# Kernel optimization log

Hardware: AMD Instinct MI355X
Metric: run time of the kernel (lower is better)

## Reference

```python
import jax, jax.numpy as jnp
import numpy as np

N, E, G = 50000, 800000, 512
HD, ED, GD, HID = 128, 64, 64, 128  # h_dim, e_dim, g_dim, hid_dim


def _mlp2(x, W1, b1, W2, b2, last_act):
    # Linear -> ReLU -> Linear (-> optional last activation)
    y = jax.nn.relu(x @ W1 + b1) @ W2 + b2
    return last_act(y) if last_act is not None else y


def setup_inputs() -> dict:
    key = jax.random.key(0)
    ks = list(jax.random.split(key, 24))
    ki = iter(ks)

    def p(shape):
        return (jax.random.normal(next(ki), shape, jnp.float32) * 0.02)

    inp = {
        "h": jax.random.normal(next(ki), (N, HD), jnp.float32),
        "e_index": jax.random.randint(next(ki), (2, E), 0, N),
        "e": jax.random.normal(next(ki), (E, ED), jnp.float32),
        "g": jax.random.normal(next(ki), (G, GD), jnp.float32),
        "batch": jnp.sort(jax.random.randint(next(ki), (N,), 0, G)),
        # fc_m: [2*HD+ED+GD, HID, HID], last_activation=relu
        "W_m1": p((2 * HD + ED + GD, HID)), "b_m1": jnp.zeros((HID,), jnp.float32),
        "W_m2": p((HID, HID)), "b_m2": jnp.zeros((HID,), jnp.float32),
        # fc_m_att: [HID, 1], sigmoid
        "W_ma": p((HID, 1)), "b_ma": jnp.zeros((1,), jnp.float32),
        # fc_e: [HID, ED, ED]
        "W_e1": p((HID, ED)), "b_e1": jnp.zeros((ED,), jnp.float32),
        "W_e2": p((ED, ED)), "b_e2": jnp.zeros((ED,), jnp.float32),
        # fc_h: [HD+HID+GD, HD, HD]
        "W_h1": p((HD + HID + GD, HD)), "b_h1": jnp.zeros((HD,), jnp.float32),
        "W_h2": p((HD, HD)), "b_h2": jnp.zeros((HD,), jnp.float32),
        # fc_h_att: [HD, 1]
        "W_ha": p((HD, 1)), "b_ha": jnp.zeros((1,), jnp.float32),
        # fc_g: [GD+HD, GD, GD]
        "W_g1": p((GD + HD, GD)), "b_g1": jnp.zeros((GD,), jnp.float32),
        "W_g2": p((GD, GD)), "b_g2": jnp.zeros((GD,), jnp.float32),
    }
    return inp


def reference(h, e_index, e, g, batch,
              W_m1, b_m1, W_m2, b_m2, W_ma, b_ma,
              W_e1, b_e1, W_e2, b_e2,
              W_h1, b_h1, W_h2, b_h2, W_ha, b_ha,
              W_g1, b_g1, W_g2, b_g2):
    src, dst = e_index[0], e_index[1]
    e_batch = batch[dst]

    # edge message: concat gathered endpoints + edge feat + gathered global
    m_cat = jnp.concatenate([h[src], h[dst], e, g[e_batch]], axis=1)  # [E, 2HD+ED+GD]
    m = jax.nn.relu(jax.nn.relu(m_cat @ W_m1 + b_m1) @ W_m2 + b_m2)   # [E, HID]
    m_att = jax.nn.sigmoid(m @ W_ma + b_ma)                            # [E, 1]

    e_update = _mlp2(m, W_e1, b_e1, W_e2, b_e2, None)                  # [E, ED]
    e_out = jax.nn.relu(e + e_update)

    m_aggr = jax.ops.segment_sum(m_att * m, dst, num_segments=h.shape[0])  # [N, HID]

    h_cat = jnp.concatenate([h, m_aggr, g[batch]], axis=1)             # [N, HD+HID+GD]
    h_update = _mlp2(h_cat, W_h1, b_h1, W_h2, b_h2, None)
    h_out = jax.nn.relu(h + h_update)                                  # [N, HD]
    h_att = h_out @ W_ha + b_ha                                        # [N, 1]

    h_aggr = jax.ops.segment_sum(h_att * h_out, batch, num_segments=g.shape[0])  # [G, HD]

    g_cat = jnp.concatenate([g, h_aggr], axis=1)                       # [G, GD+HD]
    g_update = _mlp2(g_cat, W_g1, b_g1, W_g2, b_g2, None)
    g_out = jax.nn.relu(g + g_update)

    return (h_out, e_out, g_out)
```

## Files before the change

### kernel.cpp

```cpp
#include <hip/hip_runtime.h>
#include <hip/hip_bf16.h>

#define NN 50000
#define NE 800000
#define NG 512
#define HD 128
#define ED 64
#define GD 64
#define HID 128

typedef __attribute__((ext_vector_type(8))) short short8;
typedef __attribute__((ext_vector_type(4))) short short4v;
typedef __attribute__((ext_vector_type(4))) float f32x4;

__device__ __forceinline__ short f2bf(float f) {
  union { float f; unsigned u; } v; v.f = f;
  unsigned r = v.u + 0x7fffu + ((v.u >> 16) & 1u);
  return (short)(r >> 16);
}

__device__ __forceinline__ float bf2f(short s) {
  union { unsigned u; float f; } v;
  v.u = ((unsigned)(unsigned short)s) << 16;
  return v.f;
}

__device__ __forceinline__ short8 load_a8(const float* p) {
  const f32x4* q = (const f32x4*)p;
  f32x4 x0 = q[0], x1 = q[1];
  short8 r;
  r[0]=f2bf(x0[0]); r[1]=f2bf(x0[1]); r[2]=f2bf(x0[2]); r[3]=f2bf(x0[3]);
  r[4]=f2bf(x1[0]); r[5]=f2bf(x1[1]); r[6]=f2bf(x1[2]); r[7]=f2bf(x1[3]);
  return r;
}

__device__ __forceinline__ int swz(int row, int col, int rowBytes) {
  int b = row * rowBytes + col * 2;
  b ^= (row & 7) << 4;
  return b >> 1;
}

__global__ void pack_kernel(const float* __restrict__ Wm1, const float* __restrict__ Wm2,
                            const float* __restrict__ We1, const float* __restrict__ We2,
                            const float* __restrict__ Wh1, const float* __restrict__ Wh2,
                            short* __restrict__ out) {
  int gid = blockIdx.x * 256 + threadIdx.x;
  if (gid >= 135168) return;
  const float* W; int Ncol, base, idx;
  if (gid < 49152)       { W = Wm1; Ncol = 128; base = 0;      idx = gid; }
  else if (gid < 65536)  { W = Wm2; Ncol = 128; base = 49152;  idx = gid - 49152; }
  else if (gid < 73728)  { W = We1; Ncol = 64;  base = 65536;  idx = gid - 65536; }
  else if (gid < 77824)  { W = We2; Ncol = 64;  base = 73728;  idx = gid - 73728; }
  else if (gid < 118784) { W = Wh1; Ncol = 128; base = 77824;  idx = gid - 77824; }
  else                   { W = Wh2; Ncol = 128; base = 118784; idx = gid - 118784; }
  int k = idx / Ncol, n = idx % Ncol;
  out[base + (k >> 3) * Ncol * 8 + n * 8 + (k & 7)] = f2bf(W[idx]);
}

__global__ void cast_kernel(const float* __restrict__ h, const float* __restrict__ g,
                            short* __restrict__ h_bf, short* __restrict__ g_bf) {
  int gid = blockIdx.x * 256 + threadIdx.x;
  const int H4 = NN * HD / 4;
  const int G4 = NG * GD / 4;
  if (gid < H4) {
    f32x4 v = ((const f32x4*)h)[gid];
    short4v r; r[0]=f2bf(v[0]); r[1]=f2bf(v[1]); r[2]=f2bf(v[2]); r[3]=f2bf(v[3]);
    *(short4v*)(h_bf + gid * 4) = r;
  } else if (gid < H4 + G4) {
    int i = gid - H4;
    f32x4 v = ((const f32x4*)g)[i];
    short4v r; r[0]=f2bf(v[0]); r[1]=f2bf(v[1]); r[2]=f2bf(v[2]); r[3]=f2bf(v[3]);
    *(short4v*)(g_bf + i * 4) = r;
  }
}

__global__ void count_kernel(const int* __restrict__ ei, int* __restrict__ deg) {
  int i = blockIdx.x * 256 + threadIdx.x;
  if (i < NE) atomicAdd(&deg[ei[NE + i]], 1);
}

__global__ __launch_bounds__(1024) void scan_kernel(int* __restrict__ deg) {
  __shared__ int psum[1024];
  const int CH = 49;
  int t = threadIdx.x;
  int lo = t * CH, hi = lo + CH; if (hi > NN) hi = NN; if (lo > NN) lo = NN;
  int s = 0;
  for (int i = lo; i < hi; ++i) s += deg[i];
  psum[t] = s;
  __syncthreads();
  for (int d = 1; d < 1024; d <<= 1) {
    int v = (t >= d) ? psum[t - d] : 0;
    __syncthreads();
    psum[t] += v;
    __syncthreads();
  }
  int run = (t == 0) ? 0 : psum[t - 1];
  for (int i = lo; i < hi; ++i) { int v = deg[i]; deg[i] = run; run += v; }
}

__global__ void scatter_kernel(const int* __restrict__ ei, int* __restrict__ off,
                               int* __restrict__ elist) {
  int i = blockIdx.x * 256 + threadIdx.x;
  if (i < NE) {
    int d = ei[NE + i];
    int p = atomicAdd(&off[d], 1);
    elist[p] = i;
  }
}

__global__ __launch_bounds__(256) void edge_kernel(
    const short* __restrict__ h_bf, const int* __restrict__ ei,
    const float* __restrict__ e, const short* __restrict__ g_bf,
    const int* __restrict__ batch, const int* __restrict__ elist,
    const short* __restrict__ pWm1, const float* __restrict__ bm1,
    const short* __restrict__ pWm2, const float* __restrict__ bm2,
    const float* __restrict__ Wma, const float* __restrict__ bma,
    const short* __restrict__ pWe1, const float* __restrict__ be1,
    const short* __restrict__ pWe2, const float* __restrict__ be2,
    float* __restrict__ e_out, float* __restrict__ m_aggr) {
  __shared__ short lds_m[4][16 * 128];
  __shared__ short lds_t[4][16 * 64];
  __shared__ int sdst[64];

  const int wave = threadIdx.x >> 6;
  const int lane = threadIdx.x & 63;
  const int row16 = lane & 15;
  const int quad = lane >> 4;
  const int pbase = blockIdx.x * 64 + wave * 16;

  const int eidA = elist[pbase + row16];
  const int srcA = ei[eidA];
  const int dstA = ei[NE + eidA];
  const int gbA = batch[dstA];
  if (quad == 0) sdst[wave * 16 + row16] = dstA;

  int eidS[4];
#pragma unroll
  for (int r = 0; r < 4; ++r) eidS[r] = elist[pbase + quad * 4 + r];

  short8 afr[12];
  {
    const short* s0 = h_bf + (size_t)srcA * HD;
    const short* s1 = h_bf + (size_t)dstA * HD;
    const float* s2 = e + (size_t)eidA * ED;
    const short* s3 = g_bf + (size_t)gbA * GD;
#pragma unroll
    for (int c = 0; c < 4; ++c) afr[c] = *(const short8*)(s0 + c * 32 + quad * 8);
#pragma unroll
    for (int c = 0; c < 4; ++c) afr[4 + c] = *(const short8*)(s1 + c * 32 + quad * 8);
    afr[8] = load_a8(s2 + quad * 8);
    afr[9] = load_a8(s2 + 32 + quad * 8);
    afr[10] = *(const short8*)(s3 + quad * 8);
    afr[11] = *(const short8*)(s3 + 32 + quad * 8);
  }

  float eres[4][4];
#pragma unroll
  for (int t = 0; t < 4; ++t)
#pragma unroll
    for (int r = 0; r < 4; ++r)
      eres[t][r] = e[(size_t)eidS[r] * ED + t * 16 + row16];

  f32x4 acc[8];
#pragma unroll
  for (int t = 0; t < 8; ++t) acc[t] = (f32x4)0.0f;
#pragma unroll
  for (int c = 0; c < 12; ++c) {
    const short* bp = pWm1 + (size_t)(c * 4 + quad) * HID * 8 + row16 * 8;
#pragma unroll
    for (int t = 0; t < 8; ++t) {
      short8 b = *(const short8*)(bp + t * 16 * 8);
      acc[t] = __builtin_amdgcn_mfma_f32_16x16x32_bf16(afr[c], b, acc[t], 0, 0, 0);
    }
  }
#pragma unroll
  for (int t = 0; t < 8; ++t) {
    float b1 = bm1[t * 16 + row16];
#pragma unroll
    for (int r = 0; r < 4; ++r) {
      float y = fmaxf(acc[t][r] + b1, 0.f);
      lds_m[wave][swz(quad * 4 + r, t * 16 + row16, 256)] = f2bf(y);
    }
  }

  f32x4 acc2[8];
#pragma unroll
  for (int t = 0; t < 8; ++t) acc2[t] = (f32x4)0.0f;
#pragma unroll
  for (int c = 0; c < 4; ++c) {
    short8 a = *(const short8*)&lds_m[wave][swz(row16, c * 32 + quad * 8, 256)];
    const short* bp = pWm2 + (size_t)(c * 4 + quad) * HID * 8 + row16 * 8;
#pragma unroll
    for (int t = 0; t < 8; ++t) {
      short8 b = *(const short8*)(bp + t * 16 * 8);
      acc2[t] = __builtin_amdgcn_mfma_f32_16x16x32_bf16(a, b, acc2[t], 0, 0, 0);
    }
  }

  float mval[8][4];
#pragma unroll
  for (int t = 0; t < 8; ++t) {
    float b2 = bm2[t * 16 + row16];
#pragma unroll
    for (int r = 0; r < 4; ++r) {
      float y = fmaxf(acc2[t][r] + b2, 0.f);
      mval[t][r] = y;
      lds_m[wave][swz(quad * 4 + r, t * 16 + row16, 256)] = f2bf(y);
    }
  }

  float part[4] = {0.f, 0.f, 0.f, 0.f};
#pragma unroll
  for (int t = 0; t < 8; ++t) {
    float w = Wma[t * 16 + row16];
#pragma unroll
    for (int r = 0; r < 4; ++r) part[r] += mval[t][r] * w;
  }
#pragma unroll
  for (int s = 1; s < 16; s <<= 1) {
#pragma unroll
    for (int r = 0; r < 4; ++r) part[r] += __shfl_xor(part[r], s, 64);
  }
  float bma0 = bma[0];
  float attv[4];
#pragma unroll
  for (int r = 0; r < 4; ++r) attv[r] = 1.f / (1.f + __expf(-(part[r] + bma0)));

  f32x4 acc3[4];
#pragma unroll
  for (int t = 0; t < 4; ++t) acc3[t] = (f32x4)0.0f;
#pragma unroll
  for (int c = 0; c < 4; ++c) {
    short8 a = *(const short8*)&lds_m[wave][swz(row16, c * 32 + quad * 8, 256)];
    const short* bp = pWe1 + (size_t)(c * 4 + quad) * ED * 8 + row16 * 8;
#pragma unroll
    for (int t = 0; t < 4; ++t) {
      short8 b = *(const short8*)(bp + t * 16 * 8);
      acc3[t] = __builtin_amdgcn_mfma_f32_16x16x32_bf16(a, b, acc3[t], 0, 0, 0);
    }
  }
#pragma unroll
  for (int t = 0; t < 4; ++t) {
    float b1 = be1[t * 16 + row16];
#pragma unroll
    for (int r = 0; r < 4; ++r) {
      float y = fmaxf(acc3[t][r] + b1, 0.f);
      lds_t[wave][swz(quad * 4 + r, t * 16 + row16, 128)] = f2bf(y);
    }
  }

#pragma unroll
  for (int t = 0; t < 8; ++t)
#pragma unroll
    for (int r = 0; r < 4; ++r)
      lds_m[wave][swz(quad * 4 + r, t * 16 + row16, 256)] = f2bf(attv[r] * mval[t][r]);

  f32x4 acc4[4];
#pragma unroll
  for (int t = 0; t < 4; ++t) acc4[t] = (f32x4)0.0f;
#pragma unroll
  for (int c = 0; c < 2; ++c) {
    short8 a = *(const short8*)&lds_t[wave][swz(row16, c * 32 + quad * 8, 128)];
    const short* bp = pWe2 + (size_t)(c * 4 + quad) * ED * 8 + row16 * 8;
#pragma unroll
    for (int t = 0; t < 4; ++t) {
      short8 b = *(const short8*)(bp + t * 16 * 8);
      acc4[t] = __builtin_amdgcn_mfma_f32_16x16x32_bf16(a, b, acc4[t], 0, 0, 0);
    }
  }
#pragma unroll
  for (int t = 0; t < 4; ++t) {
    float b2 = be2[t * 16 + row16];
#pragma unroll
    for (int r = 0; r < 4; ++r) {
      int col = t * 16 + row16;
      float v = eres[t][r] + acc4[t][r] + b2;
      e_out[(size_t)eidS[r] * ED + col] = fmaxf(v, 0.f);
    }
  }

  __syncthreads();

  {
    int col = threadIdx.x & 127;
    int r0 = (threadIdx.x >> 7) * 32;
    int cur = sdst[r0];
    float sum = 0.f;
    bool first = true;
#pragma unroll 1
    for (int r = r0; r < r0 + 32; ++r) {
      int d = sdst[r];
      float v = bf2f(lds_m[r >> 4][swz(r & 15, col, 256)]);
      if (d != cur) {
        if (first) atomicAdd(&m_aggr[(size_t)cur * HID + col], sum);
        else m_aggr[(size_t)cur * HID + col] = sum;
        first = false; cur = d; sum = v;
      } else {
        sum += v;
      }
    }
    atomicAdd(&m_aggr[(size_t)cur * HID + col], sum);
  }
}

__global__ __launch_bounds__(256) void node_kernel(
    const float* __restrict__ h, const short* __restrict__ h_bf,
    const float* __restrict__ m_aggr, const short* __restrict__ g_bf,
    const int* __restrict__ batch,
    const short* __restrict__ pWh1, const float* __restrict__ bh1,
    const short* __restrict__ pWh2, const float* __restrict__ bh2,
    const float* __restrict__ Wha, const float* __restrict__ bha,
    float* __restrict__ h_out, float* __restrict__ h_aggr) {
  __shared__ short lds_y[4][16 * 128];
  __shared__ int sbat[64];

  const int wave = threadIdx.x >> 6;
  const int lane = threadIdx.x & 63;
  const int row16 = lane & 15;
  const int quad = lane >> 4;
  const int nbase = blockIdx.x * 64 + wave * 16;

  int nA = nbase + row16;
  int nAc = nA < NN ? nA : NN - 1;
  int gbA = batch[nAc];
  if (quad == 0) sbat[wave * 16 + row16] = (nA < NN) ? gbA : -1;

  short8 afr[10];
  {
    const short* s0 = h_bf + (size_t)nAc * HD;
    const float* s1 = m_aggr + (size_t)nAc * HID;
    const short* s2 = g_bf + (size_t)gbA * GD;
#pragma unroll
    for (int c = 0; c < 4; ++c) afr[c] = *(const short8*)(s0 + c * 32 + quad * 8);
#pragma unroll
    for (int c = 0; c < 4; ++c) afr[4 + c] = load_a8(s1 + c * 32 + quad * 8);
    afr[8] = *(const short8*)(s2 + quad * 8);
    afr[9] = *(const short8*)(s2 + 32 + quad * 8);
  }

  f32x4 acc[8];
#pragma unroll
  for (int t = 0; t < 8; ++t) acc[t] = (f32x4)0.0f;
#pragma unroll
  for (int c = 0; c < 10; ++c) {
    const short* bp = pWh1 + (size_t)(c * 4 + quad) * HD * 8 + row16 * 8;
#pragma unroll
    for (int t = 0; t < 8; ++t) {
      short8 b = *(const short8*)(bp + t * 16 * 8);
      acc[t] = __builtin_amdgcn_mfma_f32_16x16x32_bf16(afr[c], b, acc[t], 0, 0, 0);
    }
  }
#pragma unroll
  for (int t = 0; t < 8; ++t) {
    float b1 = bh1[t * 16 + row16];
#pragma unroll
    for (int r = 0; r < 4; ++r) {
      float y = fmaxf(acc[t][r] + b1, 0.f);
      lds_y[wave][swz(quad * 4 + r, t * 16 + row16, 256)] = f2bf(y);
    }
  }

  f32x4 acc2[8];
#pragma unroll
  for (int t = 0; t < 8; ++t) acc2[t] = (f32x4)0.0f;
#pragma unroll
  for (int c = 0; c < 4; ++c) {
    short8 a = *(const short8*)&lds_y[wave][swz(row16, c * 32 + quad * 8, 256)];
    const short* bp = pWh2 + (size_t)(c * 4 + quad) * HD * 8 + row16 * 8;
#pragma unroll
    for (int t = 0; t < 8; ++t) {
      short8 b = *(const short8*)(bp + t * 16 * 8);
      acc2[t] = __builtin_amdgcn_mfma_f32_16x16x32_bf16(a, b, acc2[t], 0, 0, 0);
    }
  }

  float hval[8][4];
  int nS[4];
#pragma unroll
  for (int r = 0; r < 4; ++r) nS[r] = nbase + quad * 4 + r;
#pragma unroll
  for (int t = 0; t < 8; ++t) {
    float b2 = bh2[t * 16 + row16];
#pragma unroll
    for (int r = 0; r < 4; ++r) {
      float v = 0.f;
      if (nS[r] < NN) {
        v = h[(size_t)nS[r] * HD + t * 16 + row16] + acc2[t][r] + b2;
        v = fmaxf(v, 0.f);
        h_out[(size_t)nS[r] * HD + t * 16 + row16] = v;
      }
      hval[t][r] = v;
    }
  }

  float part[4] = {0.f, 0.f, 0.f, 0.f};
#pragma unroll
  for (int t = 0; t < 8; ++t) {
    float w = Wha[t * 16 + row16];
#pragma unroll
    for (int r = 0; r < 4; ++r) part[r] += hval[t][r] * w;
  }
#pragma unroll
  for (int s = 1; s < 16; s <<= 1) {
#pragma unroll
    for (int r = 0; r < 4; ++r) part[r] += __shfl_xor(part[r], s, 64);
  }
  float bha0 = bha[0];
#pragma unroll
  for (int t = 0; t < 8; ++t)
#pragma unroll
    for (int r = 0; r < 4; ++r)
      lds_y[wave][swz(quad * 4 + r, t * 16 + row16, 256)] =
          f2bf((part[r] + bha0) * hval[t][r]);

  __syncthreads();

  {
    int col = threadIdx.x & 127;
    int r0 = (threadIdx.x >> 7) * 32;
    int cur = sbat[r0];
    float sum = 0.f;
    bool first = true;
#pragma unroll 1
    for (int r = r0; r < r0 + 32; ++r) {
      int d = sbat[r];
      float v = bf2f(lds_y[r >> 4][swz(r & 15, col, 256)]);
      if (d != cur) {
        if (cur >= 0) {
          if (first) atomicAdd(&h_aggr[(size_t)cur * HD + col], sum);
          else h_aggr[(size_t)cur * HD + col] = sum;
        }
        first = false; cur = d; sum = v;
      } else {
        sum += v;
      }
    }
    if (cur >= 0) atomicAdd(&h_aggr[(size_t)cur * HD + col], sum);
  }
}

__global__ void g_kernel(const float* __restrict__ g, const float* __restrict__ h_aggr,
                         const float* __restrict__ Wg1, const float* __restrict__ bg1,
                         const float* __restrict__ Wg2, const float* __restrict__ bg2,
                         float* __restrict__ g_out) {
  __shared__ float cat[192];
  __shared__ float y1[64];
  int r = blockIdx.x;
  int t = threadIdx.x;
  cat[t] = g[(size_t)r * GD + t];
  cat[64 + t] = h_aggr[(size_t)r * HD + t];
  cat[128 + t] = h_aggr[(size_t)r * HD + 64 + t];
  __syncthreads();
  float a = bg1[t];
  for (int k = 0; k < 192; ++k) a += cat[k] * Wg1[k * 64 + t];
  y1[t] = fmaxf(a, 0.f);
  __syncthreads();
  float b = bg2[t];
  for (int k = 0; k < 64; ++k) b += y1[k] * Wg2[k * 64 + t];
  float v = g[(size_t)r * GD + t] + b;
  g_out[(size_t)r * GD + t] = fmaxf(v, 0.f);
}

extern "C" void kernel_launch(void* const* d_in, const int* in_sizes, int n_in,
                              void* d_out, int out_size, void* d_ws, size_t ws_size,
                              hipStream_t stream) {
  const float* h = (const float*)d_in[0];
  const int* ei = (const int*)d_in[1];
  const float* e = (const float*)d_in[2];
  const float* g = (const float*)d_in[3];
  const int* batch = (const int*)d_in[4];
  const float* Wm1 = (const float*)d_in[5];
  const float* bm1 = (const float*)d_in[6];
  const float* Wm2 = (const float*)d_in[7];
  const float* bm2 = (const float*)d_in[8];
  const float* Wma = (const float*)d_in[9];
  const float* bma = (const float*)d_in[10];
  const float* We1 = (const float*)d_in[11];
  const float* be1 = (const float*)d_in[12];
  const float* We2 = (const float*)d_in[13];
  const float* be2 = (const float*)d_in[14];
  const float* Wh1 = (const float*)d_in[15];
  const float* bh1 = (const float*)d_in[16];
  const float* Wh2 = (const float*)d_in[17];
  const float* bh2 = (const float*)d_in[18];
  const float* Wha = (const float*)d_in[19];
  const float* bha = (const float*)d_in[20];
  const float* Wg1 = (const float*)d_in[21];
  const float* bg1 = (const float*)d_in[22];
  const float* Wg2 = (const float*)d_in[23];
  const float* bg2 = (const float*)d_in[24];

  float* out = (float*)d_out;
  float* h_out = out;
  float* e_out = out + (size_t)NN * HD;
  float* g_out = e_out + (size_t)NE * ED;

  char* ws = (char*)d_ws;
  float* m_aggr = (float*)ws;
  float* h_aggr = (float*)(ws + 25600000);
  short* packed = (short*)(ws + 25862144);
  int* deg      = (int*)(ws + 26132480);
  int* elist    = (int*)(ws + 26332480);
  short* h_bf   = (short*)(ws + 29532480);
  short* g_bf   = (short*)(ws + 42332480);
  short* pWm1 = packed;
  short* pWm2 = packed + 49152;
  short* pWe1 = packed + 65536;
  short* pWe2 = packed + 73728;
  short* pWh1 = packed + 77824;
  short* pWh2 = packed + 118784;

  hipMemsetAsync(m_aggr, 0, (size_t)NN * HID * 4, stream);
  hipMemsetAsync(h_aggr, 0, (size_t)NG * HD * 4, stream);
  hipMemsetAsync(deg, 0, (size_t)NN * 4, stream);

  pack_kernel<<<(135168 + 255) / 256, 256, 0, stream>>>(Wm1, Wm2, We1, We2, Wh1, Wh2, packed);
  cast_kernel<<<(1608192 + 255) / 256, 256, 0, stream>>>(h, g, h_bf, g_bf);
  count_kernel<<<(NE + 255) / 256, 256, 0, stream>>>(ei, deg);
  scan_kernel<<<1, 1024, 0, stream>>>(deg);
  scatter_kernel<<<(NE + 255) / 256, 256, 0, stream>>>(ei, deg, elist);

  edge_kernel<<<NE / 64, 256, 0, stream>>>(h_bf, ei, e, g_bf, batch, elist,
                                           pWm1, bm1, pWm2, bm2, Wma, bma,
                                           pWe1, be1, pWe2, be2, e_out, m_aggr);

  node_kernel<<<(NN + 63) / 64, 256, 0, stream>>>(h, h_bf, m_aggr, g_bf, batch,
                                                  pWh1, bh1, pWh2, bh2, Wha, bha,
                                                  h_out, h_aggr);

  g_kernel<<<NG, 64, 0, stream>>>(g, h_aggr, Wg1, bg1, Wg2, bg2, g_out);
}
```

Baseline: 728.7 us.

## Retile edge kernel to 256 edges per block with 32x32 MFMA

Rewrites the edge kernel to process 256 edges per block, each wave covering 64 rows with 32x32x16 bf16 MFMAs instead of 16x16x32. This lets each weight fragment loaded from memory feed two row tiles, which reduces weight traffic per edge. Attention scaling moves into the segment-sum pass, which now runs over 128-row runs and so issues fewer atomics. The second e-MLP layer is deferred until after the aggregation, reusing the same LDS buffer. The cost is much higher register pressure (a launch bound of 2 blocks) and a larger LDS footprint per block, which may reduce occupancy.

```diff
diff --git a/kernel.cpp b/kernel.cpp
--- a/kernel.cpp
+++ b/kernel.cpp
@@ -8,10 +8,12 @@
 #define ED 64
 #define GD 64
 #define HID 128
+#define EB 256
 
 typedef __attribute__((ext_vector_type(8))) short short8;
 typedef __attribute__((ext_vector_type(4))) short short4v;
 typedef __attribute__((ext_vector_type(4))) float f32x4;
+typedef __attribute__((ext_vector_type(16))) float f32x16;
 
 __device__ __forceinline__ short f2bf(float f) {
   union { float f; unsigned u; } v; v.f = f;
@@ -108,7 +110,7 @@
   }
 }
 
-__global__ __launch_bounds__(256) void edge_kernel(
+__global__ __launch_bounds__(256, 2) void edge_kernel(
     const short* __restrict__ h_bf, const int* __restrict__ ei,
     const float* __restrict__ e, const short* __restrict__ g_bf,
     const int* __restrict__ batch, const int* __restrict__ elist,
@@ -118,179 +120,176 @@
     const short* __restrict__ pWe1, const float* __restrict__ be1,
     const short* __restrict__ pWe2, const float* __restrict__ be2,
     float* __restrict__ e_out, float* __restrict__ m_aggr) {
-  __shared__ short lds_m[4][16 * 128];
-  __shared__ short lds_t[4][16 * 64];
-  __shared__ int sdst[64];
-
-  const int wave = threadIdx.x >> 6;
-  const int lane = threadIdx.x & 63;
-  const int row16 = lane & 15;
-  const int quad = lane >> 4;
-  const int pbase = blockIdx.x * 64 + wave * 16;
-
-  const int eidA = elist[pbase + row16];
-  const int srcA = ei[eidA];
-  const int dstA = ei[NE + eidA];
-  const int gbA = batch[dstA];
-  if (quad == 0) sdst[wave * 16 + row16] = dstA;
-
-  int eidS[4];
-#pragma unroll
-  for (int r = 0; r < 4; ++r) eidS[r] = elist[pbase + quad * 4 + r];
-
-  short8 afr[12];
+  __shared__ short lds_m[EB * 128];
+  __shared__ float att_s[EB];
+  __shared__ int sdst[EB];
+  __shared__ int seid[EB];
+  short* ebuf = lds_m;
+
+  const int tid = threadIdx.x;
+  const int w = tid >> 6;
+  const int l = tid & 63;
+  const int c32 = l & 31;
+  const int hi = l >> 5;
+  const int eb = blockIdx.x * EB;
+
   {
-    const short* s0 = h_bf + (size_t)srcA * HD;
-    const short* s1 = h_bf + (size_t)dstA * HD;
-    const float* s2 = e + (size_t)eidA * ED;
-    const short* s3 = g_bf + (size_t)gbA * GD;
-#pragma unroll
-    for (int c = 0; c < 4; ++c) afr[c] = *(const short8*)(s0 + c * 32 + quad * 8);
-#pragma unroll
-    for (int c = 0; c < 4; ++c) afr[4 + c] = *(const short8*)(s1 + c * 32 + quad * 8);
-    afr[8] = load_a8(s2 + quad * 8);
-    afr[9] = load_a8(s2 + 32 + quad * 8);
-    afr[10] = *(const short8*)(s3 + quad * 8);
-    afr[11] = *(const short8*)(s3 + 32 + quad * 8);
-  }
-
-  float eres[4][4];
-#pragma unroll
-  for (int t = 0; t < 4; ++t)
-#pragma unroll
-    for (int r = 0; r < 4; ++r)
-      eres[t][r] = e[(size_t)eidS[r] * ED + t * 16 + row16];
-
-  f32x4 acc[8];
-#pragma unroll
-  for (int t = 0; t < 8; ++t) acc[t] = (f32x4)0.0f;
-#pragma unroll
-  for (int c = 0; c < 12; ++c) {
-    const short* bp = pWm1 + (size_t)(c * 4 + quad) * HID * 8 + row16 * 8;
-#pragma unroll
-    for (int t = 0; t < 8; ++t) {
-      short8 b = *(const short8*)(bp + t * 16 * 8);
-      acc[t] = __builtin_amdgcn_mfma_f32_16x16x32_bf16(afr[c], b, acc[t], 0, 0, 0);
-    }
-  }
-#pragma unroll
-  for (int t = 0; t < 8; ++t) {
-    float b1 = bm1[t * 16 + row16];
-#pragma unroll
-    for (int r = 0; r < 4; ++r) {
-      float y = fmaxf(acc[t][r] + b1, 0.f);
-      lds_m[wave][swz(quad * 4 + r, t * 16 + row16, 256)] = f2bf(y);
-    }
-  }
-
-  f32x4 acc2[8];
-#pragma unroll
-  for (int t = 0; t < 8; ++t) acc2[t] = (f32x4)0.0f;
-#pragma unroll
-  for (int c = 0; c < 4; ++c) {
-    short8 a = *(const short8*)&lds_m[wave][swz(row16, c * 32 + quad * 8, 256)];
-    const short* bp = pWm2 + (size_t)(c * 4 + quad) * HID * 8 + row16 * 8;
-#pragma unroll
-    for (int t = 0; t < 8; ++t) {
-      short8 b = *(const short8*)(bp + t * 16 * 8);
-      acc2[t] = __builtin_amdgcn_mfma_f32_16x16x32_bf16(a, b, acc2[t], 0, 0, 0);
-    }
-  }
-
-  float mval[8][4];
-#pragma unroll
-  for (int t = 0; t < 8; ++t) {
-    float b2 = bm2[t * 16 + row16];
-#pragma unroll
-    for (int r = 0; r < 4; ++r) {
-      float y = fmaxf(acc2[t][r] + b2, 0.f);
-      mval[t][r] = y;
-      lds_m[wave][swz(quad * 4 + r, t * 16 + row16, 256)] = f2bf(y);
-    }
-  }
-
-  float part[4] = {0.f, 0.f, 0.f, 0.f};
-#pragma unroll
-  for (int t = 0; t < 8; ++t) {
-    float w = Wma[t * 16 + row16];
-#pragma unroll
-    for (int r = 0; r < 4; ++r) part[r] += mval[t][r] * w;
-  }
-#pragma unroll
-  for (int s = 1; s < 16; s <<= 1) {
-#pragma unroll
-    for (int r = 0; r < 4; ++r) part[r] += __shfl_xor(part[r], s, 64);
-  }
-  float bma0 = bma[0];
-  float attv[4];
-#pragma unroll
-  for (int r = 0; r < 4; ++r) attv[r] = 1.f / (1.f + __expf(-(part[r] + bma0)));
-
-  f32x4 acc3[4];
-#pragma unroll
-  for (int t = 0; t < 4; ++t) acc3[t] = (f32x4)0.0f;
-#pragma unroll
-  for (int c = 0; c < 4; ++c) {
-    short8 a = *(const short8*)&lds_m[wave][swz(row16, c * 32 + quad * 8, 256)];
-    const short* bp = pWe1 + (size_t)(c * 4 + quad) * ED * 8 + row16 * 8;
+    int eid = elist[eb + tid];
+    seid[tid] = eid;
+    sdst[tid] = ei[NE + eid];
+  }
+
+  int eidr[2], srcr[2], dstr[2], gbr[2];
+#pragma unroll
+  for (int rt = 0; rt < 2; ++rt) {
+    int row = w * 64 + rt * 32 + c32;
+    int eid = seid[row];
+    eidr[rt] = eid;
+    dstr[rt] = sdst[row];
+    srcr[rt] = ei[eid];
+    gbr[rt] = batch[dstr[rt]];
+  }
+
+  f32x16 acc[2][4];
+#pragma unroll
+  for (int rt = 0; rt < 2; ++rt)
+#pragma unroll
+    for (int t = 0; t < 4; ++t) acc[rt][t] = (f32x16)0.0f;
+
+#pragma unroll
+  for (int kk = 0; kk < 24; ++kk) {
+    short8 a[2];
+#pragma unroll
+    for (int rt = 0; rt < 2; ++rt) {
+      if (kk < 8)
+        a[rt] = *(const short8*)(h_bf + (size_t)srcr[rt] * HD + kk * 16 + hi * 8);
+      else if (kk < 16)
+        a[rt] = *(const short8*)(h_bf + (size_t)dstr[rt] * HD + (kk - 8) * 16 + hi * 8);
+      else if (kk < 20)
+        a[rt] = load_a8(e + (size_t)eidr[rt] * ED + (kk - 16) * 16 + hi * 8);
+      else
+        a[rt] = *(const short8*)(g_bf + (size_t)gbr[rt] * GD + (kk - 20) * 16 + hi * 8);
+    }
+    const short* bp = pWm1 + (size_t)(kk * 2 + hi) * (HID * 8) + c32 * 8;
 #pragma unroll
     for (int t = 0; t < 4; ++t) {
-      short8 b = *(const short8*)(bp + t * 16 * 8);
-      acc3[t] = __builtin_amdgcn_mfma_f32_16x16x32_bf16(a, b, acc3[t], 0, 0, 0);
-    }
-  }
-#pragma unroll
-  for (int t = 0; t < 4; ++t) {
-    float b1 = be1[t * 16 + row16];
-#pragma unroll
-    for (int r = 0; r < 4; ++r) {
-      float y = fmaxf(acc3[t][r] + b1, 0.f);
-      lds_t[wave][swz(quad * 4 + r, t * 16 + row16, 128)] = f2bf(y);
-    }
-  }
-
-#pragma unroll
-  for (int t = 0; t < 8; ++t)
-#pragma unroll
-    for (int r = 0; r < 4; ++r)
-      lds_m[wave][swz(quad * 4 + r, t * 16 + row16, 256)] = f2bf(attv[r] * mval[t][r]);
-
-  f32x4 acc4[4];
-#pragma unroll
-  for (int t = 0; t < 4; ++t) acc4[t] = (f32x4)0.0f;
-#pragma unroll
-  for (int c = 0; c < 2; ++c) {
-    short8 a = *(const short8*)&lds_t[wave][swz(row16, c * 32 + quad * 8, 128)];
-    const short* bp = pWe2 + (size_t)(c * 4 + quad) * ED * 8 + row16 * 8;
+      short8 b = *(const short8*)(bp + t * 32 * 8);
+#pragma unroll
+      for (int rt = 0; rt < 2; ++rt)
+        acc[rt][t] = __builtin_amdgcn_mfma_f32_32x32x16_bf16(a[rt], b, acc[rt][t], 0, 0, 0);
+    }
+  }
+
+#pragma unroll
+  for (int rt = 0; rt < 2; ++rt)
 #pragma unroll
     for (int t = 0; t < 4; ++t) {
-      short8 b = *(const short8*)(bp + t * 16 * 8);
-      acc4[t] = __builtin_amdgcn_mfma_f32_16x16x32_bf16(a, b, acc4[t], 0, 0, 0);
-    }
-  }
-#pragma unroll
-  for (int t = 0; t < 4; ++t) {
-    float b2 = be2[t * 16 + row16];
-#pragma unroll
-    for (int r = 0; r < 4; ++r) {
-      int col = t * 16 + row16;
-      float v = eres[t][r] + acc4[t][r] + b2;
-      e_out[(size_t)eidS[r] * ED + col] = fmaxf(v, 0.f);
+      float bb = bm1[t * 32 + c32];
+#pragma unroll
+      for (int q = 0; q < 16; ++q) {
+        int row = w * 64 + rt * 32 + (q & 3) + 8 * (q >> 2) + 4 * hi;
+        float y = fmaxf(acc[rt][t][q] + bb, 0.f);
+        lds_m[swz(row, t * 32 + c32, 256)] = f2bf(y);
+      }
+    }
+
+  f32x16 acc2[2][4];
+#pragma unroll
+  for (int rt = 0; rt < 2; ++rt)
+#pragma unroll
+    for (int t = 0; t < 4; ++t) acc2[rt][t] = (f32x16)0.0f;
+
+#pragma unroll
+  for (int ks = 0; ks < 8; ++ks) {
+    short8 a[2];
+#pragma unroll
+    for (int rt = 0; rt < 2; ++rt)
+      a[rt] = *(const short8*)&lds_m[swz(w * 64 + rt * 32 + c32, ks * 16 + hi * 8, 256)];
+    const short* bp = pWm2 + (size_t)(ks * 2 + hi) * (HID * 8) + c32 * 8;
+#pragma unroll
+    for (int t = 0; t < 4; ++t) {
+      short8 b = *(const short8*)(bp + t * 32 * 8);
+#pragma unroll
+      for (int rt = 0; rt < 2; ++rt)
+        acc2[rt][t] = __builtin_amdgcn_mfma_f32_32x32x16_bf16(a[rt], b, acc2[rt][t], 0, 0, 0);
+    }
+  }
+
+  float p[2][16];
+#pragma unroll
+  for (int rt = 0; rt < 2; ++rt)
+#pragma unroll
+    for (int q = 0; q < 16; ++q) p[rt][q] = 0.f;
+
+#pragma unroll
+  for (int rt = 0; rt < 2; ++rt)
+#pragma unroll
+    for (int t = 0; t < 4; ++t) {
+      float bb = bm2[t * 32 + c32];
+      float wv = Wma[t * 32 + c32];
+#pragma unroll
+      for (int q = 0; q < 16; ++q) {
+        int row = w * 64 + rt * 32 + (q & 3) + 8 * (q >> 2) + 4 * hi;
+        float y = fmaxf(acc2[rt][t][q] + bb, 0.f);
+        lds_m[swz(row, t * 32 + c32, 256)] = f2bf(y);
+        p[rt][q] += y * wv;
+      }
+    }
+
+#pragma unroll
+  for (int s = 1; s <= 16; s <<= 1) {
+#pragma unroll
+    for (int rt = 0; rt < 2; ++rt)
+#pragma unroll
+      for (int q = 0; q < 16; ++q) p[rt][q] += __shfl_xor(p[rt][q], s, 64);
+  }
+  {
+    float bma0 = bma[0];
+    if (c32 == 0) {
+#pragma unroll
+      for (int rt = 0; rt < 2; ++rt)
+#pragma unroll
+        for (int q = 0; q < 16; ++q) {
+          int row = w * 64 + rt * 32 + (q & 3) + 8 * (q >> 2) + 4 * hi;
+          att_s[row] = 1.f / (1.f + __expf(-(p[rt][q] + bma0)));
+        }
+    }
+  }
+
+  f32x16 acc3[2][2];
+#pragma unroll
+  for (int rt = 0; rt < 2; ++rt)
+#pragma unroll
+    for (int t = 0; t < 2; ++t) acc3[rt][t] = (f32x16)0.0f;
+
+#pragma unroll
+  for (int ks = 0; ks < 8; ++ks) {
+    short8 a[2];
+#pragma unroll
+    for (int rt = 0; rt < 2; ++rt)
+      a[rt] = *(const short8*)&lds_m[swz(w * 64 + rt * 32 + c32, ks * 16 + hi * 8, 256)];
+    const short* bp = pWe1 + (size_t)(ks * 2 + hi) * (ED * 8) + c32 * 8;
+#pragma unroll
+    for (int t = 0; t < 2; ++t) {
+      short8 b = *(const short8*)(bp + t * 32 * 8);
+#pragma unroll
+      for (int rt = 0; rt < 2; ++rt)
+        acc3[rt][t] = __builtin_amdgcn_mfma_f32_32x32x16_bf16(a[rt], b, acc3[rt][t], 0, 0, 0);
     }
   }
 
   __syncthreads();
 
   {
-    int col = threadIdx.x & 127;
-    int r0 = (threadIdx.x >> 7) * 32;
+    int col = tid & 127;
+    int r0 = (tid >> 7) * 128;
     int cur = sdst[r0];
     float sum = 0.f;
     bool first = true;
 #pragma unroll 1
-    for (int r = r0; r < r0 + 32; ++r) {
+    for (int r = r0; r < r0 + 128; ++r) {
       int d = sdst[r];
-      float v = bf2f(lds_m[r >> 4][swz(r & 15, col, 256)]);
+      float v = bf2f(lds_m[swz(r, col, 256)]) * att_s[r];
       if (d != cur) {
         if (first) atomicAdd(&m_aggr[(size_t)cur * HID + col], sum);
         else m_aggr[(size_t)cur * HID + col] = sum;
@@ -301,6 +300,58 @@
     }
     atomicAdd(&m_aggr[(size_t)cur * HID + col], sum);
   }
+
+  __syncthreads();
+
+#pragma unroll
+  for (int rt = 0; rt < 2; ++rt)
+#pragma unroll
+    for (int t = 0; t < 2; ++t) {
+      float bb = be1[t * 32 + c32];
+#pragma unroll
+      for (int q = 0; q < 16; ++q) {
+        int row = w * 64 + rt * 32 + (q & 3) + 8 * (q >> 2) + 4 * hi;
+        float y = fmaxf(acc3[rt][t][q] + bb, 0.f);
+        ebuf[swz(row, t * 32 + c32, 128)] = f2bf(y);
+      }
+    }
+
+  f32x16 acc4[2][2];
+#pragma unroll
+  for (int rt = 0; rt < 2; ++rt)
+#pragma unroll
+    for (int t = 0; t < 2; ++t) acc4[rt][t] = (f32x16)0.0f;
+
+#pragma unroll
+  for (int ks = 0; ks < 4; ++ks) {
+    short8 a[2];
+#pragma unroll
+    for (int rt = 0; rt < 2; ++rt)
+      a[rt] = *(const short8*)&ebuf[swz(w * 64 + rt * 32 + c32, ks * 16 + hi * 8, 128)];
+    const short* bp = pWe2 + (size_t)(ks * 2 + hi) * (ED * 8) + c32 * 8;
+#pragma unroll
+    for (int t = 0; t < 2; ++t) {
+      short8 b = *(const short8*)(bp + t * 32 * 8);
+#pragma unroll
+      for (int rt = 0; rt < 2; ++rt)
+        acc4[rt][t] = __builtin_amdgcn_mfma_f32_32x32x16_bf16(a[rt], b, acc4[rt][t], 0, 0, 0);
+    }
+  }
+
+#pragma unroll
+  for (int rt = 0; rt < 2; ++rt)
+#pragma unroll
+    for (int t = 0; t < 2; ++t) {
+      float bb = be2[t * 32 + c32];
+#pragma unroll
+      for (int q = 0; q < 16; ++q) {
+        int row = w * 64 + rt * 32 + (q & 3) + 8 * (q >> 2) + 4 * hi;
+        int eid = seid[row];
+        int col = t * 32 + c32;
+        float v = e[(size_t)eid * ED + col] + acc4[rt][t][q] + bb;
+        e_out[(size_t)eid * ED + col] = fmaxf(v, 0.f);
+      }
+    }
 }
 
 __global__ __launch_bounds__(256) void node_kernel(
@@ -520,7 +571,7 @@
   scan_kernel<<<1, 1024, 0, stream>>>(deg);
   scatter_kernel<<<(NE + 255) / 256, 256, 0, stream>>>(ei, deg, elist);
 
-  edge_kernel<<<NE / 64, 256, 0, stream>>>(h_bf, ei, e, g_bf, batch, elist,
+  edge_kernel<<<NE / EB, 256, 0, stream>>>(h_bf, ei, e, g_bf, batch, elist,
                                            pWm1, bm1, pWm2, bm2, Wma, bma,
                                            pWe1, be1, pWe2, be2, e_out, m_aggr);
 
```

Result: slower. 940.6 us (+29.1%).

## Pre-cast edge features to bf16 and slim edge kernel register and LDS use

Applied to the files above, without the earlier changes.

Edge features are now converted to bf16 in the cast kernel, which also absorbs the degree-count pass, so one launch is removed. The edge kernel no longer preloads all twelve A fragments, the fp32 residual or the m values into registers. It loads A fragments per chunk, keeps attention weights in LDS and uses a single shared LDS buffer for m and the e-MLP hidden layer, all to cut VGPR and LDS pressure and raise occupancy. The segment aggregation now runs earlier and applies attention on the fly with paired columns. The cost is an extra full pass over the edge features plus a bf16 copy written to and read back from memory. The e_out residual also now uses bf16-rounded e, which lowers accuracy.

```diff
diff --git a/kernel.cpp b/kernel.cpp
--- a/kernel.cpp
+++ b/kernel.cpp
@@ -8,9 +8,11 @@
 #define ED 64
 #define GD 64
 #define HID 128
+#define EB 64
 
 typedef __attribute__((ext_vector_type(8))) short short8;
 typedef __attribute__((ext_vector_type(4))) short short4v;
+typedef __attribute__((ext_vector_type(2))) float f32x2;
 typedef __attribute__((ext_vector_type(4))) float f32x4;
 
 __device__ __forceinline__ short f2bf(float f) {
@@ -58,10 +60,13 @@
 }
 
 __global__ void cast_kernel(const float* __restrict__ h, const float* __restrict__ g,
-                            short* __restrict__ h_bf, short* __restrict__ g_bf) {
+                            const float* __restrict__ e, const int* __restrict__ ei,
+                            short* __restrict__ h_bf, short* __restrict__ g_bf,
+                            short* __restrict__ e_bf, int* __restrict__ deg) {
   int gid = blockIdx.x * 256 + threadIdx.x;
   const int H4 = NN * HD / 4;
   const int G4 = NG * GD / 4;
+  const int E4 = NE * ED / 4;
   if (gid < H4) {
     f32x4 v = ((const f32x4*)h)[gid];
     short4v r; r[0]=f2bf(v[0]); r[1]=f2bf(v[1]); r[2]=f2bf(v[2]); r[3]=f2bf(v[3]);
@@ -71,12 +76,15 @@
     f32x4 v = ((const f32x4*)g)[i];
     short4v r; r[0]=f2bf(v[0]); r[1]=f2bf(v[1]); r[2]=f2bf(v[2]); r[3]=f2bf(v[3]);
     *(short4v*)(g_bf + i * 4) = r;
-  }
-}
-
-__global__ void count_kernel(const int* __restrict__ ei, int* __restrict__ deg) {
-  int i = blockIdx.x * 256 + threadIdx.x;
-  if (i < NE) atomicAdd(&deg[ei[NE + i]], 1);
+  } else if (gid < H4 + G4 + E4) {
+    int i = gid - H4 - G4;
+    f32x4 v = ((const f32x4*)e)[i];
+    short4v r; r[0]=f2bf(v[0]); r[1]=f2bf(v[1]); r[2]=f2bf(v[2]); r[3]=f2bf(v[3]);
+    *(short4v*)(e_bf + i * 4) = r;
+  } else if (gid < H4 + G4 + E4 + NE) {
+    int i = gid - H4 - G4 - E4;
+    atomicAdd(&deg[ei[NE + i]], 1);
+  }
 }
 
 __global__ __launch_bounds__(1024) void scan_kernel(int* __restrict__ deg) {
@@ -110,7 +118,7 @@
 
 __global__ __launch_bounds__(256) void edge_kernel(
     const short* __restrict__ h_bf, const int* __restrict__ ei,
-    const float* __restrict__ e, const short* __restrict__ g_bf,
+    const short* __restrict__ e_bf, const short* __restrict__ g_bf,
     const int* __restrict__ batch, const int* __restrict__ elist,
     const short* __restrict__ pWm1, const float* __restrict__ bm1,
     const short* __restrict__ pWm2, const float* __restrict__ bm2,
@@ -118,59 +126,51 @@
     const short* __restrict__ pWe1, const float* __restrict__ be1,
     const short* __restrict__ pWe2, const float* __restrict__ be2,
     float* __restrict__ e_out, float* __restrict__ m_aggr) {
-  __shared__ short lds_m[4][16 * 128];
-  __shared__ short lds_t[4][16 * 64];
-  __shared__ int sdst[64];
-
-  const int wave = threadIdx.x >> 6;
-  const int lane = threadIdx.x & 63;
+  __shared__ short lds_m[EB * 128];
+  __shared__ float att_s[EB];
+  __shared__ int sdst[EB];
+  __shared__ int seid[EB];
+  short* ebuf = lds_m;
+
+  const int tid = threadIdx.x;
+  const int w = tid >> 6;
+  const int lane = tid & 63;
   const int row16 = lane & 15;
   const int quad = lane >> 4;
-  const int pbase = blockIdx.x * 64 + wave * 16;
-
-  const int eidA = elist[pbase + row16];
-  const int srcA = ei[eidA];
-  const int dstA = ei[NE + eidA];
-  const int gbA = batch[dstA];
-  if (quad == 0) sdst[wave * 16 + row16] = dstA;
-
-  int eidS[4];
-#pragma unroll
-  for (int r = 0; r < 4; ++r) eidS[r] = elist[pbase + quad * 4 + r];
-
-  short8 afr[12];
-  {
-    const short* s0 = h_bf + (size_t)srcA * HD;
-    const short* s1 = h_bf + (size_t)dstA * HD;
-    const float* s2 = e + (size_t)eidA * ED;
-    const short* s3 = g_bf + (size_t)gbA * GD;
-#pragma unroll
-    for (int c = 0; c < 4; ++c) afr[c] = *(const short8*)(s0 + c * 32 + quad * 8);
-#pragma unroll
-    for (int c = 0; c < 4; ++c) afr[4 + c] = *(const short8*)(s1 + c * 32 + quad * 8);
-    afr[8] = load_a8(s2 + quad * 8);
-    afr[9] = load_a8(s2 + 32 + quad * 8);
-    afr[10] = *(const short8*)(s3 + quad * 8);
-    afr[11] = *(const short8*)(s3 + 32 + quad * 8);
-  }
-
-  float eres[4][4];
-#pragma unroll
-  for (int t = 0; t < 4; ++t)
-#pragma unroll
-    for (int r = 0; r < 4; ++r)
-      eres[t][r] = e[(size_t)eidS[r] * ED + t * 16 + row16];
+  const int eb = blockIdx.x * EB;
+
+  if (tid < EB) {
+    int eid = elist[eb + tid];
+    seid[tid] = eid;
+    sdst[tid] = ei[NE + eid];
+  }
+
+  const int eidr = elist[eb + w * 16 + row16];
+  const int dstr = ei[NE + eidr];
+  const int srcr = ei[eidr];
+  const int gbr = batch[dstr];
+
+  const short* seg0 = h_bf + (size_t)srcr * HD;
+  const short* seg1 = h_bf + (size_t)dstr * HD;
+  const short* seg2 = e_bf + (size_t)eidr * ED;
+  const short* seg3 = g_bf + (size_t)gbr * GD;
 
   f32x4 acc[8];
 #pragma unroll
   for (int t = 0; t < 8; ++t) acc[t] = (f32x4)0.0f;
 #pragma unroll
   for (int c = 0; c < 12; ++c) {
-    const short* bp = pWm1 + (size_t)(c * 4 + quad) * HID * 8 + row16 * 8;
+    const short* src; int off;
+    if (c < 4)       { src = seg0; off = c * 32; }
+    else if (c < 8)  { src = seg1; off = (c - 4) * 32; }
+    else if (c < 10) { src = seg2; off = (c - 8) * 32; }
+    else             { src = seg3; off = (c - 10) * 32; }
+    short8 a = *(const short8*)(src + off + quad * 8);
+    const short* bp = pWm1 + (size_t)(c * 4 + quad) * (HID * 8) + row16 * 8;
 #pragma unroll
     for (int t = 0; t < 8; ++t) {
       short8 b = *(const short8*)(bp + t * 16 * 8);
-      acc[t] = __builtin_amdgcn_mfma_f32_16x16x32_bf16(afr[c], b, acc[t], 0, 0, 0);
+      acc[t] = __builtin_amdgcn_mfma_f32_16x16x32_bf16(a, b, acc[t], 0, 0, 0);
     }
   }
 #pragma unroll
@@ -179,7 +179,7 @@
 #pragma unroll
     for (int r = 0; r < 4; ++r) {
       float y = fmaxf(acc[t][r] + b1, 0.f);
-      lds_m[wave][swz(quad * 4 + r, t * 16 + row16, 256)] = f2bf(y);
+      lds_m[swz(w * 16 + quad * 4 + r, t * 16 + row16, 256)] = f2bf(y);
     }
   }
 
@@ -188,8 +188,8 @@
   for (int t = 0; t < 8; ++t) acc2[t] = (f32x4)0.0f;
 #pragma unroll
   for (int c = 0; c < 4; ++c) {
-    short8 a = *(const short8*)&lds_m[wave][swz(row16, c * 32 + quad * 8, 256)];
-    const short* bp = pWm2 + (size_t)(c * 4 + quad) * HID * 8 + row16 * 8;
+    short8 a = *(const short8*)&lds_m[swz(w * 16 + row16, c * 32 + quad * 8, 256)];
+    const short* bp = pWm2 + (size_t)(c * 4 + quad) * (HID * 8) + row16 * 8;
 #pragma unroll
     for (int t = 0; t < 8; ++t) {
       short8 b = *(const short8*)(bp + t * 16 * 8);
@@ -197,109 +197,118 @@
     }
   }
 
-  float mval[8][4];
+  float p[4] = {0.f, 0.f, 0.f, 0.f};
 #pragma unroll
   for (int t = 0; t < 8; ++t) {
     float b2 = bm2[t * 16 + row16];
+    float wv = Wma[t * 16 + row16];
 #pragma unroll
     for (int r = 0; r < 4; ++r) {
       float y = fmaxf(acc2[t][r] + b2, 0.f);
-      mval[t][r] = y;
-      lds_m[wave][swz(quad * 4 + r, t * 16 + row16, 256)] = f2bf(y);
-    }
-  }
-
-  float part[4] = {0.f, 0.f, 0.f, 0.f};
-#pragma unroll
-  for (int t = 0; t < 8; ++t) {
-    float w = Wma[t * 16 + row16];
-#pragma unroll
-    for (int r = 0; r < 4; ++r) part[r] += mval[t][r] * w;
-  }
+      lds_m[swz(w * 16 + quad * 4 + r, t * 16 + row16, 256)] = f2bf(y);
+      p[r] += y * wv;
+    }
+  }
+
 #pragma unroll
   for (int s = 1; s < 16; s <<= 1) {
 #pragma unroll
-    for (int r = 0; r < 4; ++r) part[r] += __shfl_xor(part[r], s, 64);
-  }
-  float bma0 = bma[0];
-  float attv[4];
-#pragma unroll
-  for (int r = 0; r < 4; ++r) attv[r] = 1.f / (1.f + __expf(-(part[r] + bma0)));
+    for (int r = 0; r < 4; ++r) p[r] += __shfl_xor(p[r], s, 64);
+  }
+  {
+    float bma0 = bma[0];
+    if (row16 == 0) {
+#pragma unroll
+      for (int r = 0; r < 4; ++r)
+        att_s[w * 16 + quad * 4 + r] = 1.f / (1.f + __expf(-(p[r] + bma0)));
+    }
+  }
 
   f32x4 acc3[4];
 #pragma unroll
   for (int t = 0; t < 4; ++t) acc3[t] = (f32x4)0.0f;
 #pragma unroll
   for (int c = 0; c < 4; ++c) {
-    short8 a = *(const short8*)&lds_m[wave][swz(row16, c * 32 + quad * 8, 256)];
-    const short* bp = pWe1 + (size_t)(c * 4 + quad) * ED * 8 + row16 * 8;
+    short8 a = *(const short8*)&lds_m[swz(w * 16 + row16, c * 32 + quad * 8, 256)];
+    const short* bp = pWe1 + (size_t)(c * 4 + quad) * (ED * 8) + row16 * 8;
 #pragma unroll
     for (int t = 0; t < 4; ++t) {
       short8 b = *(const short8*)(bp + t * 16 * 8);
       acc3[t] = __builtin_amdgcn_mfma_f32_16x16x32_bf16(a, b, acc3[t], 0, 0, 0);
     }
   }
+
+  __syncthreads();
+
+  {
+    int cp = tid & 63;
+    int r0 = (tid >> 6) * 16;
+    int cur = sdst[r0];
+    float s0 = 0.f, s1 = 0.f;
+    bool first = true;
+#pragma unroll 1
+    for (int r = r0; r < r0 + 16; ++r) {
+      int d = sdst[r];
+      unsigned u = *(const unsigned*)&lds_m[swz(r, cp * 2, 256)];
+      float av = att_s[r];
+      float v0 = bf2f((short)(u & 0xffffu)) * av;
+      float v1 = bf2f((short)(u >> 16)) * av;
+      if (d != cur) {
+        if (first) {
+          atomicAdd(&m_aggr[(size_t)cur * HID + cp * 2], s0);
+          atomicAdd(&m_aggr[(size_t)cur * HID + cp * 2 + 1], s1);
+        } else {
+          f32x2 st; st[0] = s0; st[1] = s1;
+          *(f32x2*)&m_aggr[(size_t)cur * HID + cp * 2] = st;
+        }
+        first = false; cur = d; s0 = v0; s1 = v1;
+      } else {
+        s0 += v0; s1 += v1;
+      }
+    }
+    atomicAdd(&m_aggr[(size_t)cur * HID + cp * 2], s0);
+    atomicAdd(&m_aggr[(size_t)cur * HID + cp * 2 + 1], s1);
+  }
+
+  __syncthreads();
+
 #pragma unroll
   for (int t = 0; t < 4; ++t) {
     float b1 = be1[t * 16 + row16];
 #pragma unroll
     for (int r = 0; r < 4; ++r) {
       float y = fmaxf(acc3[t][r] + b1, 0.f);
-      lds_t[wave][swz(quad * 4 + r, t * 16 + row16, 128)] = f2bf(y);
-    }
-  }
-
-#pragma unroll
-  for (int t = 0; t < 8; ++t)
-#pragma unroll
-    for (int r = 0; r < 4; ++r)
-      lds_m[wave][swz(quad * 4 + r, t * 16 + row16, 256)] = f2bf(attv[r] * mval[t][r]);
+      ebuf[swz(w * 16 + quad * 4 + r, t * 16 + row16, 128)] = f2bf(y);
+    }
+  }
 
   f32x4 acc4[4];
 #pragma unroll
   for (int t = 0; t < 4; ++t) acc4[t] = (f32x4)0.0f;
 #pragma unroll
   for (int c = 0; c < 2; ++c) {
-    short8 a = *(const short8*)&lds_t[wave][swz(row16, c * 32 + quad * 8, 128)];
-    const short* bp = pWe2 + (size_t)(c * 4 + quad) * ED * 8 + row16 * 8;
+    short8 a = *(const short8*)&ebuf[swz(w * 16 + row16, c * 32 + quad * 8, 128)];
+    const short* bp = pWe2 + (size_t)(c * 4 + quad) * (ED * 8) + row16 * 8;
 #pragma unroll
     for (int t = 0; t < 4; ++t) {
       short8 b = *(const short8*)(bp + t * 16 * 8);
       acc4[t] = __builtin_amdgcn_mfma_f32_16x16x32_bf16(a, b, acc4[t], 0, 0, 0);
     }
   }
+
+  int eidS[4];
+#pragma unroll
+  for (int r = 0; r < 4; ++r) eidS[r] = seid[w * 16 + quad * 4 + r];
 #pragma unroll
   for (int t = 0; t < 4; ++t) {
     float b2 = be2[t * 16 + row16];
 #pragma unroll
     for (int r = 0; r < 4; ++r) {
       int col = t * 16 + row16;
-      float v = eres[t][r] + acc4[t][r] + b2;
+      float res = bf2f(e_bf[(size_t)eidS[r] * ED + col]);
+      float v = res + acc4[t][r] + b2;
       e_out[(size_t)eidS[r] * ED + col] = fmaxf(v, 0.f);
     }
-  }
-
-  __syncthreads();
-
-  {
-    int col = threadIdx.x & 127;
-    int r0 = (threadIdx.x >> 7) * 32;
-    int cur = sdst[r0];
-    float sum = 0.f;
-    bool first = true;
-#pragma unroll 1
-    for (int r = r0; r < r0 + 32; ++r) {
-      int d = sdst[r];
-      float v = bf2f(lds_m[r >> 4][swz(r & 15, col, 256)]);
-      if (d != cur) {
-        if (first) atomicAdd(&m_aggr[(size_t)cur * HID + col], sum);
-        else m_aggr[(size_t)cur * HID + col] = sum;
-        first = false; cur = d; sum = v;
-      } else {
-        sum += v;
-      }
-    }
-    atomicAdd(&m_aggr[(size_t)cur * HID + col], sum);
   }
 }
 
@@ -503,6 +512,7 @@
   int* elist    = (int*)(ws + 26332480);
   short* h_bf   = (short*)(ws + 29532480);
   short* g_bf   = (short*)(ws + 42332480);
+  short* e_bf   = (short*)(ws + 42398016);
   short* pWm1 = packed;
   short* pWm2 = packed + 49152;
   short* pWe1 = packed + 65536;
@@ -515,12 +525,11 @@
   hipMemsetAsync(deg, 0, (size_t)NN * 4, stream);
 
   pack_kernel<<<(135168 + 255) / 256, 256, 0, stream>>>(Wm1, Wm2, We1, We2, Wh1, Wh2, packed);
-  cast_kernel<<<(1608192 + 255) / 256, 256, 0, stream>>>(h, g, h_bf, g_bf);
-  count_kernel<<<(NE + 255) / 256, 256, 0, stream>>>(ei, deg);
+  cast_kernel<<<(15208192 + 255) / 256, 256, 0, stream>>>(h, g, e, ei, h_bf, g_bf, e_bf, deg);
   scan_kernel<<<1, 1024, 0, stream>>>(deg);
   scatter_kernel<<<(NE + 255) / 256, 256, 0, stream>>>(ei, deg, elist);
 
-  edge_kernel<<<NE / 64, 256, 0, stream>>>(h_bf, ei, e, g_bf, batch, elist,
+  edge_kernel<<<NE / EB, 256, 0, stream>>>(h_bf, ei, e_bf, g_bf, batch, elist,
                                            pWm1, bm1, pWm2, bm2, Wma, bma,
                                            pWe1, be1, pWe2, be2, e_out, m_aggr);
 
```

After: 690.0 us. 5.3% less time.
